# Kernel tuning notes

Hardware: AMD Instinct MI355X
Metric: run time of the kernel (lower is better)

Reference implementation:

```python
import jax, jax.numpy as jnp
import numpy as np

N, IN_C, HID, E = 100000, 1024, 128, 1600000


def setup_inputs() -> dict:
    key = jax.random.key(0)
    k1, k2, k3 = jax.random.split(key, 3)
    x = jax.random.normal(k1, (N, IN_C), dtype=jnp.float32)
    # GCNConv weight (bias=False), applied as x @ W : [in, hidden]
    W = jax.random.normal(k2, (IN_C, HID), dtype=jnp.float32) * (1.0 / np.sqrt(IN_C))
    edge_index = jax.random.randint(k3, (2, E), 0, N, dtype=jnp.int64)
    return {"x": x, "W": W, "edge_index": edge_index}


def reference(x, W, edge_index):
    n = x.shape[0]
    row, col = edge_index[0], edge_index[1]  # src -> dst
    # add self-loops (PyG GCNConv default)
    loop = jnp.arange(n, dtype=edge_index.dtype)
    row = jnp.concatenate([row, loop])
    col = jnp.concatenate([col, loop])
    # symmetric normalization: deg on destination, includes self-loops (deg >= 1)
    deg = jax.ops.segment_sum(jnp.ones(col.shape, jnp.float32), col, num_segments=n)
    dinv = jax.lax.rsqrt(deg)
    norm = dinv[row] * dinv[col]  # [E+N]
    # linear transform first (in -> hidden), then gather/scale/scatter-add
    h = x @ W                      # [N, HID]
    msg = h[row] * norm[:, None]   # [E+N, HID]
    out = jax.ops.segment_sum(msg, col, num_segments=n)  # [N, HID]
    return out
```

## Files before the change

### kernel.cpp

```cpp
#include <hip/hip_runtime.h>
#include <hip/hip_bf16.h>

#define NN 100000
#define INC 1024
#define HID 128
#define NE 1600000
#define NB ((NN + 255) / 256)

typedef float floatx4 __attribute__((ext_vector_type(4)));
typedef __bf16 bf16x8 __attribute__((ext_vector_type(8)));
typedef unsigned short ushort8v __attribute__((ext_vector_type(8)));
typedef unsigned short ushort4v __attribute__((ext_vector_type(4)));

__device__ __forceinline__ unsigned short f2bf(float f) {
    union { float f; unsigned u; } v; v.f = f;
    unsigned r = v.u + 0x7fffu + ((v.u >> 16) & 1u);
    return (unsigned short)(r >> 16);
}

__global__ __launch_bounds__(256) void init_cnt_k(int* cnt) {
    int i = blockIdx.x * 256 + threadIdx.x;
    if (i < NN) cnt[i] = 0;
}

__global__ __launch_bounds__(256) void deg_edges_k(const int* __restrict__ col, int* cnt) {
    int e = blockIdx.x * 256 + threadIdx.x;
    if (e < NE) atomicAdd(&cnt[col[e]], 1);
}

__global__ __launch_bounds__(256) void dinv_k(const int* __restrict__ cnt, float* __restrict__ dinv) {
    int i = blockIdx.x * 256 + threadIdx.x;
    if (i < NN) dinv[i] = rsqrtf((float)(cnt[i] + 1));
}

__global__ __launch_bounds__(256) void scan1_k(const int* __restrict__ cnt,
                                               int* __restrict__ excl, int* __restrict__ bsum) {
    __shared__ int sh[256];
    const int t = threadIdx.x, b = blockIdx.x;
    const int idx = b * 256 + t;
    const int v = (idx < NN) ? cnt[idx] : 0;
    sh[t] = v;
    __syncthreads();
#pragma unroll
    for (int off = 1; off < 256; off <<= 1) {
        const int x = sh[t];
        const int y = (t >= off) ? sh[t - off] : 0;
        __syncthreads();
        sh[t] = x + y;
        __syncthreads();
    }
    if (idx < NN) excl[idx] = sh[t] - v;
    if (t == 255) bsum[b] = sh[255];
}

__global__ __launch_bounds__(512) void scan2_k(const int* __restrict__ bsum, int* __restrict__ boff) {
    __shared__ int sh[512];
    const int t = threadIdx.x;
    const int v = (t < NB) ? bsum[t] : 0;
    sh[t] = v;
    __syncthreads();
#pragma unroll
    for (int off = 1; off < 512; off <<= 1) {
        const int x = sh[t];
        const int y = (t >= off) ? sh[t - off] : 0;
        __syncthreads();
        sh[t] = x + y;
        __syncthreads();
    }
    if (t < NB) boff[t] = sh[t] - v;
}

__global__ __launch_bounds__(256) void scan3_k(const int* __restrict__ excl, const int* __restrict__ boff,
                                               int* __restrict__ rowptr, int* __restrict__ cursor) {
    const int idx = blockIdx.x * 256 + threadIdx.x;
    if (idx < NN) {
        const int v = excl[idx] + boff[blockIdx.x];
        rowptr[idx] = v;
        cursor[idx] = v;
    }
    if (idx == 0) rowptr[NN] = NE;
}

__global__ __launch_bounds__(256) void fill_k(const int* __restrict__ ei,
                                              int* cursor, int* __restrict__ ssrc) {
    const int e = blockIdx.x * 256 + threadIdx.x;
    if (e < NE) {
        const int r = ei[e];
        const int c = ei[NE + e];
        const int pos = atomicAdd(&cursor[c], 1);
        ssrc[pos] = r;
    }
}

__global__ __launch_bounds__(256) void wt_k(const float* __restrict__ W, unsigned short* __restrict__ Wt) {
    int idx = blockIdx.x * 256 + threadIdx.x;
    int n = idx >> 10, k = idx & 1023;
    Wt[idx] = f2bf(W[k * HID + n]);
}

__global__ __launch_bounds__(256) void gemm_hp_k(
    const float* __restrict__ x, const unsigned short* __restrict__ Wt,
    const float* __restrict__ dinv, float* __restrict__ hp)
{
    __shared__ unsigned short As[64 * 40];
    __shared__ unsigned short Bs[128 * 40];
    const int tid  = threadIdx.x;
    const int lane = tid & 63;
    const int wave = tid >> 6;
    const int q    = lane >> 4;
    const int l16  = lane & 15;
    const int brow = blockIdx.x * 64;

    floatx4 acc[8];
#pragma unroll
    for (int t = 0; t < 8; ++t) acc[t] = (floatx4){0.f, 0.f, 0.f, 0.f};

    for (int k0 = 0; k0 < INC; k0 += 32) {
        {
            const int m  = tid >> 3;
            const int kk = (tid & 7) * 4;
#pragma unroll
            for (int h = 0; h < 2; ++h) {
                const int mm = m + h * 32;
                const int g  = brow + mm;
                float4 v = make_float4(0.f, 0.f, 0.f, 0.f);
                if (g < NN) v = *(const float4*)&x[(size_t)g * INC + k0 + kk];
                ushort4v w;
                w.x = f2bf(v.x); w.y = f2bf(v.y); w.z = f2bf(v.z); w.w = f2bf(v.w);
                *(ushort4v*)&As[mm * 40 + kk] = w;
            }
        }
        {
            const int n  = tid >> 1;
            const int kk = (tid & 1) * 16;
            ushort8v a = *(const ushort8v*)&Wt[(size_t)n * INC + k0 + kk];
            ushort8v b = *(const ushort8v*)&Wt[(size_t)n * INC + k0 + kk + 8];
            *(ushort8v*)&Bs[n * 40 + kk]     = a;
            *(ushort8v*)&Bs[n * 40 + kk + 8] = b;
        }
        __syncthreads();

        const bf16x8 af = *(const bf16x8*)&As[(wave * 16 + l16) * 40 + q * 8];
#pragma unroll
        for (int t = 0; t < 8; ++t) {
            const bf16x8 bf = *(const bf16x8*)&Bs[(t * 16 + l16) * 40 + q * 8];
            acc[t] = __builtin_amdgcn_mfma_f32_16x16x32_bf16(af, bf, acc[t], 0, 0, 0);
        }
        __syncthreads();
    }

#pragma unroll
    for (int r = 0; r < 4; ++r) {
        const int row = brow + wave * 16 + q * 4 + r;
        if (row < NN) {
            const float d = dinv[row];
#pragma unroll
            for (int t = 0; t < 8; ++t) {
                const int col = t * 16 + l16;
                hp[(size_t)row * HID + col] = acc[t][r] * d;
            }
        }
    }
}

__global__ __launch_bounds__(256) void agg_k(const int* __restrict__ rowptr,
                                             const int* __restrict__ ssrc,
                                             const float* __restrict__ hp,
                                             const float* __restrict__ dinv,
                                             float* __restrict__ out)
{
    const int w = (blockIdx.x * 256 + threadIdx.x) >> 6;
    const int lane = threadIdx.x & 63;
    if (w >= NN) return;
    const int s = rowptr[w];
    const int e = rowptr[w + 1];
    const size_t loff = (size_t)lane * 2;

    const float2 self = *(const float2*)&hp[(size_t)w * HID + loff];
    float ax = self.x, ay = self.y;

    for (int i = s; i < e; i += 64) {
        const int rem = e - i;
        const int cnt = rem < 64 ? rem : 64;
        int srcv = 0;
        if (lane < rem) srcv = ssrc[i + lane];
        int j = 0;
        for (; j + 4 <= cnt; j += 4) {
            const int s0 = __shfl(srcv, j + 0);
            const int s1 = __shfl(srcv, j + 1);
            const int s2 = __shfl(srcv, j + 2);
            const int s3 = __shfl(srcv, j + 3);
            const float2 v0 = *(const float2*)&hp[(size_t)s0 * HID + loff];
            const float2 v1 = *(const float2*)&hp[(size_t)s1 * HID + loff];
            const float2 v2 = *(const float2*)&hp[(size_t)s2 * HID + loff];
            const float2 v3 = *(const float2*)&hp[(size_t)s3 * HID + loff];
            ax += v0.x + v1.x + v2.x + v3.x;
            ay += v0.y + v1.y + v2.y + v3.y;
        }
        for (; j < cnt; ++j) {
            const int sj = __shfl(srcv, j);
            const float2 v = *(const float2*)&hp[(size_t)sj * HID + loff];
            ax += v.x;
            ay += v.y;
        }
    }

    const float d = dinv[w];
    float2 r;
    r.x = ax * d;
    r.y = ay * d;
    *(float2*)&out[(size_t)w * HID + loff] = r;
}

extern "C" void kernel_launch(void* const* d_in, const int* in_sizes, int n_in,
                              void* d_out, int out_size, void* d_ws, size_t ws_size,
                              hipStream_t stream) {
    const float* x  = (const float*)d_in[0];
    const float* W  = (const float*)d_in[1];
    const int*   ei = (const int*)d_in[2];
    float* out = (float*)d_out;

    char* p = (char*)d_ws;
    float* hp      = (float*)p;            p += (size_t)NN * HID * 4;
    int*   cnt     = (int*)p;              p += (size_t)NN * 4;
    int*   rowptr  = (int*)p;              p += (size_t)(NN + 4) * 4;
    int*   cursor  = (int*)p;              p += (size_t)NN * 4;
    int*   excl    = (int*)p;              p += (size_t)NN * 4;
    float* dinv    = (float*)p;            p += (size_t)NN * 4;
    unsigned short* Wt = (unsigned short*)p; p += (size_t)INC * HID * 2;
    int*   bsum    = (int*)p;              p += 512 * 4;
    int*   boff    = (int*)p;              p += 512 * 4;
    int*   ssrc    = (int*)p;              p += (size_t)NE * 4;

    init_cnt_k <<<NB, 256, 0, stream>>>(cnt);
    deg_edges_k<<<(NE + 255) / 256, 256, 0, stream>>>(ei + NE, cnt);
    dinv_k     <<<NB, 256, 0, stream>>>(cnt, dinv);
    scan1_k    <<<NB, 256, 0, stream>>>(cnt, excl, bsum);
    scan2_k    <<<1, 512, 0, stream>>>(bsum, boff);
    scan3_k    <<<NB, 256, 0, stream>>>(excl, boff, rowptr, cursor);
    fill_k     <<<(NE + 255) / 256, 256, 0, stream>>>(ei, cursor, ssrc);
    wt_k       <<<(INC * HID) / 256, 256, 0, stream>>>(W, Wt);
    gemm_hp_k  <<<(NN + 63) / 64, 256, 0, stream>>>(x, Wt, dinv, hp);
    agg_k      <<<(NN * 64 + 255) / 256, 256, 0, stream>>>(rowptr, ssrc, hp, dinv, out);
}
```

Baseline: 923.5 us.

## Store hp in bf16, double-buffer GEMM LDS, and fuse small setup kernels

The intermediate hp matrix is now stored as bf16 rather than fp32, which halves the bytes fetched by the random-gather aggregation. The GEMM now double-buffers LDS with register prefetch of the next K tile and needs only one barrier per iteration. The W transpose is merged into the count-init kernel and the dinv computation into scan1, which removes two launches. The bf16 storage adds rounding error to the aggregated output.

```diff
diff --git a/kernel.cpp b/kernel.cpp
--- a/kernel.cpp
+++ b/kernel.cpp
@@ -18,9 +18,24 @@
     return (unsigned short)(r >> 16);
 }
 
-__global__ __launch_bounds__(256) void init_cnt_k(int* cnt) {
-    int i = blockIdx.x * 256 + threadIdx.x;
-    if (i < NN) cnt[i] = 0;
+__device__ __forceinline__ float bf_lo(unsigned u) {
+    union { unsigned u; float f; } v; v.u = u << 16; return v.f;
+}
+__device__ __forceinline__ float bf_hi(unsigned u) {
+    union { unsigned u; float f; } v; v.u = u & 0xffff0000u; return v.f;
+}
+
+__global__ __launch_bounds__(256) void init_k(int* cnt, const float* __restrict__ W,
+                                              unsigned short* __restrict__ Wt) {
+    const int b = blockIdx.x;
+    if (b < NB) {
+        const int i = b * 256 + threadIdx.x;
+        if (i < NN) cnt[i] = 0;
+    } else {
+        const int idx = (b - NB) * 256 + threadIdx.x;
+        const int n = idx >> 10, k = idx & 1023;
+        Wt[idx] = f2bf(W[k * HID + n]);
+    }
 }
 
 __global__ __launch_bounds__(256) void deg_edges_k(const int* __restrict__ col, int* cnt) {
@@ -28,13 +43,9 @@
     if (e < NE) atomicAdd(&cnt[col[e]], 1);
 }
 
-__global__ __launch_bounds__(256) void dinv_k(const int* __restrict__ cnt, float* __restrict__ dinv) {
-    int i = blockIdx.x * 256 + threadIdx.x;
-    if (i < NN) dinv[i] = rsqrtf((float)(cnt[i] + 1));
-}
-
 __global__ __launch_bounds__(256) void scan1_k(const int* __restrict__ cnt,
-                                               int* __restrict__ excl, int* __restrict__ bsum) {
+                                               int* __restrict__ excl, int* __restrict__ bsum,
+                                               float* __restrict__ dinv) {
     __shared__ int sh[256];
     const int t = threadIdx.x, b = blockIdx.x;
     const int idx = b * 256 + t;
@@ -49,7 +60,10 @@
         sh[t] = x + y;
         __syncthreads();
     }
-    if (idx < NN) excl[idx] = sh[t] - v;
+    if (idx < NN) {
+        excl[idx] = sh[t] - v;
+        dinv[idx] = rsqrtf((float)(v + 1));
+    }
     if (t == 255) bsum[b] = sh[255];
 }
 
@@ -92,18 +106,12 @@
     }
 }
 
-__global__ __launch_bounds__(256) void wt_k(const float* __restrict__ W, unsigned short* __restrict__ Wt) {
-    int idx = blockIdx.x * 256 + threadIdx.x;
-    int n = idx >> 10, k = idx & 1023;
-    Wt[idx] = f2bf(W[k * HID + n]);
-}
-
 __global__ __launch_bounds__(256) void gemm_hp_k(
     const float* __restrict__ x, const unsigned short* __restrict__ Wt,
-    const float* __restrict__ dinv, float* __restrict__ hp)
+    const float* __restrict__ dinv, unsigned short* __restrict__ hp)
 {
-    __shared__ unsigned short As[64 * 40];
-    __shared__ unsigned short Bs[128 * 40];
+    __shared__ unsigned short As[2][64 * 40];
+    __shared__ unsigned short Bs[2][128 * 40];
     const int tid  = threadIdx.x;
     const int lane = tid & 63;
     const int wave = tid >> 6;
@@ -111,42 +119,65 @@
     const int l16  = lane & 15;
     const int brow = blockIdx.x * 64;
 
+    const int am  = tid >> 3;
+    const int akk = (tid & 7) * 4;
+    const int bn  = tid >> 1;
+    const int bkk = (tid & 1) * 16;
+
     floatx4 acc[8];
 #pragma unroll
     for (int t = 0; t < 8; ++t) acc[t] = (floatx4){0.f, 0.f, 0.f, 0.f};
 
+    float4   va[2];
+    ushort8v vb[2];
+
+    {
+#pragma unroll
+        for (int h = 0; h < 2; ++h) {
+            const int g = brow + am + h * 32;
+            float4 v = make_float4(0.f, 0.f, 0.f, 0.f);
+            if (g < NN) v = *(const float4*)&x[(size_t)g * INC + akk];
+            va[h] = v;
+        }
+        vb[0] = *(const ushort8v*)&Wt[(size_t)bn * INC + bkk];
+        vb[1] = *(const ushort8v*)&Wt[(size_t)bn * INC + bkk + 8];
+    }
+
+    int buf = 0;
     for (int k0 = 0; k0 < INC; k0 += 32) {
         {
-            const int m  = tid >> 3;
-            const int kk = (tid & 7) * 4;
 #pragma unroll
             for (int h = 0; h < 2; ++h) {
-                const int mm = m + h * 32;
-                const int g  = brow + mm;
+                ushort4v w;
+                w.x = f2bf(va[h].x); w.y = f2bf(va[h].y);
+                w.z = f2bf(va[h].z); w.w = f2bf(va[h].w);
+                *(ushort4v*)&As[buf][(am + h * 32) * 40 + akk] = w;
+            }
+            *(ushort8v*)&Bs[buf][bn * 40 + bkk]     = vb[0];
+            *(ushort8v*)&Bs[buf][bn * 40 + bkk + 8] = vb[1];
+        }
+        __syncthreads();
+
+        const int kn = k0 + 32;
+        if (kn < INC) {
+#pragma unroll
+            for (int h = 0; h < 2; ++h) {
+                const int g = brow + am + h * 32;
                 float4 v = make_float4(0.f, 0.f, 0.f, 0.f);
-                if (g < NN) v = *(const float4*)&x[(size_t)g * INC + k0 + kk];
-                ushort4v w;
-                w.x = f2bf(v.x); w.y = f2bf(v.y); w.z = f2bf(v.z); w.w = f2bf(v.w);
-                *(ushort4v*)&As[mm * 40 + kk] = w;
+                if (g < NN) v = *(const float4*)&x[(size_t)g * INC + kn + akk];
+                va[h] = v;
             }
-        }
-        {
-            const int n  = tid >> 1;
-            const int kk = (tid & 1) * 16;
-            ushort8v a = *(const ushort8v*)&Wt[(size_t)n * INC + k0 + kk];
-            ushort8v b = *(const ushort8v*)&Wt[(size_t)n * INC + k0 + kk + 8];
-            *(ushort8v*)&Bs[n * 40 + kk]     = a;
-            *(ushort8v*)&Bs[n * 40 + kk + 8] = b;
-        }
-        __syncthreads();
-
-        const bf16x8 af = *(const bf16x8*)&As[(wave * 16 + l16) * 40 + q * 8];
+            vb[0] = *(const ushort8v*)&Wt[(size_t)bn * INC + kn + bkk];
+            vb[1] = *(const ushort8v*)&Wt[(size_t)bn * INC + kn + bkk + 8];
+        }
+
+        const bf16x8 af = *(const bf16x8*)&As[buf][(wave * 16 + l16) * 40 + q * 8];
 #pragma unroll
         for (int t = 0; t < 8; ++t) {
-            const bf16x8 bf = *(const bf16x8*)&Bs[(t * 16 + l16) * 40 + q * 8];
-            acc[t] = __builtin_amdgcn_mfma_f32_16x16x32_bf16(af, bf, acc[t], 0, 0, 0);
-        }
-        __syncthreads();
+            const bf16x8 bfv = *(const bf16x8*)&Bs[buf][(t * 16 + l16) * 40 + q * 8];
+            acc[t] = __builtin_amdgcn_mfma_f32_16x16x32_bf16(af, bfv, acc[t], 0, 0, 0);
+        }
+        buf ^= 1;
     }
 
 #pragma unroll
@@ -157,7 +188,7 @@
 #pragma unroll
             for (int t = 0; t < 8; ++t) {
                 const int col = t * 16 + l16;
-                hp[(size_t)row * HID + col] = acc[t][r] * d;
+                hp[(size_t)row * HID + col] = f2bf(acc[t][r] * d);
             }
         }
     }
@@ -165,7 +196,7 @@
 
 __global__ __launch_bounds__(256) void agg_k(const int* __restrict__ rowptr,
                                              const int* __restrict__ ssrc,
-                                             const float* __restrict__ hp,
+                                             const unsigned short* __restrict__ hp,
                                              const float* __restrict__ dinv,
                                              float* __restrict__ out)
 {
@@ -174,10 +205,10 @@
     if (w >= NN) return;
     const int s = rowptr[w];
     const int e = rowptr[w + 1];
-    const size_t loff = (size_t)lane * 2;
-
-    const float2 self = *(const float2*)&hp[(size_t)w * HID + loff];
-    float ax = self.x, ay = self.y;
+    const unsigned* hp32 = (const unsigned*)hp;
+
+    const unsigned uself = hp32[(size_t)w * 64 + lane];
+    float ax = bf_lo(uself), ay = bf_hi(uself);
 
     for (int i = s; i < e; i += 64) {
         const int rem = e - i;
@@ -190,18 +221,18 @@
             const int s1 = __shfl(srcv, j + 1);
             const int s2 = __shfl(srcv, j + 2);
             const int s3 = __shfl(srcv, j + 3);
-            const float2 v0 = *(const float2*)&hp[(size_t)s0 * HID + loff];
-            const float2 v1 = *(const float2*)&hp[(size_t)s1 * HID + loff];
-            const float2 v2 = *(const float2*)&hp[(size_t)s2 * HID + loff];
-            const float2 v3 = *(const float2*)&hp[(size_t)s3 * HID + loff];
-            ax += v0.x + v1.x + v2.x + v3.x;
-            ay += v0.y + v1.y + v2.y + v3.y;
+            const unsigned v0 = hp32[(size_t)s0 * 64 + lane];
+            const unsigned v1 = hp32[(size_t)s1 * 64 + lane];
+            const unsigned v2 = hp32[(size_t)s2 * 64 + lane];
+            const unsigned v3 = hp32[(size_t)s3 * 64 + lane];
+            ax += bf_lo(v0) + bf_lo(v1) + bf_lo(v2) + bf_lo(v3);
+            ay += bf_hi(v0) + bf_hi(v1) + bf_hi(v2) + bf_hi(v3);
         }
         for (; j < cnt; ++j) {
             const int sj = __shfl(srcv, j);
-            const float2 v = *(const float2*)&hp[(size_t)sj * HID + loff];
-            ax += v.x;
-            ay += v.y;
+            const unsigned v = hp32[(size_t)sj * 64 + lane];
+            ax += bf_lo(v);
+            ay += bf_hi(v);
         }
     }
 
@@ -209,7 +240,7 @@
     float2 r;
     r.x = ax * d;
     r.y = ay * d;
-    *(float2*)&out[(size_t)w * HID + loff] = r;
+    *(float2*)&out[(size_t)w * HID + (size_t)lane * 2] = r;
 }
 
 extern "C" void kernel_launch(void* const* d_in, const int* in_sizes, int n_in,
@@ -221,7 +252,7 @@
     float* out = (float*)d_out;
 
     char* p = (char*)d_ws;
-    float* hp      = (float*)p;            p += (size_t)NN * HID * 4;
+    unsigned short* hp = (unsigned short*)p; p += (size_t)NN * HID * 2;
     int*   cnt     = (int*)p;              p += (size_t)NN * 4;
     int*   rowptr  = (int*)p;              p += (size_t)(NN + 4) * 4;
     int*   cursor  = (int*)p;              p += (size_t)NN * 4;
@@ -232,14 +263,12 @@
     int*   boff    = (int*)p;              p += 512 * 4;
     int*   ssrc    = (int*)p;              p += (size_t)NE * 4;
 
-    init_cnt_k <<<NB, 256, 0, stream>>>(cnt);
+    init_k     <<<NB + (INC * HID) / 256, 256, 0, stream>>>(cnt, W, Wt);
     deg_edges_k<<<(NE + 255) / 256, 256, 0, stream>>>(ei + NE, cnt);
-    dinv_k     <<<NB, 256, 0, stream>>>(cnt, dinv);
-    scan1_k    <<<NB, 256, 0, stream>>>(cnt, excl, bsum);
+    scan1_k    <<<NB, 256, 0, stream>>>(cnt, excl, bsum, dinv);
     scan2_k    <<<1, 512, 0, stream>>>(bsum, boff);
     scan3_k    <<<NB, 256, 0, stream>>>(excl, boff, rowptr, cursor);
     fill_k     <<<(NE + 255) / 256, 256, 0, stream>>>(ei, cursor, ssrc);
-    wt_k       <<<(INC * HID) / 256, 256, 0, stream>>>(W, Wt);
     gemm_hp_k  <<<(NN + 63) / 64, 256, 0, stream>>>(x, Wt, dinv, hp);
     agg_k      <<<(NN * 64 + 255) / 256, 256, 0, stream>>>(rowptr, ssrc, hp, dinv, out);
 }
```

Result: faster. 849.3 us (-8.0%).
